# Performance work log

Measured on AMD Instinct MI355X. Metric: run time of the kernel, lower is better.

Reference implementation:

```python
import jax, jax.numpy as jnp
import numpy as np

EPS = 1e-12  # F.normalize eps


def _l2norm_c(x):
    # normalize over channel dim (axis=1), matching F.normalize(dim=1)
    n = jnp.sqrt(jnp.sum(x * x, axis=1, keepdims=True))
    return x / jnp.maximum(n, EPS)


def _rotate_all(q, angles_deg):
    """Rotate q [B,C,H,W] by every angle in angles_deg [A] via affine_grid +
    bilinear grid_sample (align_corners=False, zeros padding). Returns [A,B,C,H,W]."""
    B, C, H, W = q.shape
    th = jnp.deg2rad(angles_deg)
    # affine_grid align_corners=False output normalized coords
    xn = (2.0 * jnp.arange(W, dtype=q.dtype) + 1.0) / W - 1.0  # [W]
    yn = (2.0 * jnp.arange(H, dtype=q.dtype) + 1.0) / H - 1.0  # [H]
    c = jnp.cos(th)[:, None, None]
    s = jnp.sin(th)[:, None, None]
    gx = c * xn[None, None, :] - s * yn[None, :, None]  # [A,H,W]
    gy = s * xn[None, None, :] + c * yn[None, :, None]  # [A,H,W]
    # grid_sample align_corners=False: normalized -> input pixel coords
    ix = ((gx + 1.0) * W - 1.0) * 0.5
    iy = ((gy + 1.0) * H - 1.0) * 0.5
    x0 = jnp.floor(ix)
    y0 = jnp.floor(iy)
    wx = ix - x0  # frac weights
    wy = iy - y0
    x0i = x0.astype(jnp.int32)
    y0i = y0.astype(jnp.int32)

    def corner(yi, xi, w):
        valid = (xi >= 0) & (xi < W) & (yi >= 0) & (yi < H)  # zeros padding
        xc = jnp.clip(xi, 0, W - 1)
        yc = jnp.clip(yi, 0, H - 1)
        vals = q[:, :, yc, xc]  # advanced indexing -> [B,C,A,H,W]
        return vals * (w * valid.astype(q.dtype))[None, None]

    out = (corner(y0i, x0i, (1.0 - wx) * (1.0 - wy))
           + corner(y0i, x0i + 1, wx * (1.0 - wy))
           + corner(y0i + 1, x0i, (1.0 - wx) * wy)
           + corner(y0i + 1, x0i + 1, wx * wy))  # [B,C,A,H,W]
    return jnp.transpose(out, (2, 0, 1, 3, 4))  # [A,B,C,H,W]


def setup_inputs() -> dict:
    key = jax.random.key(0)
    ks = jax.random.split(key, 6)
    B, Cin, H, W, HID, A = 8, 768, 32, 32, 128, 36
    gallery_map = jax.random.normal(ks[0], (B, Cin, H, W), jnp.float32)
    query_map = jax.random.normal(ks[1], (B, Cin, H, W), jnp.float32)
    angles_deg = jnp.arange(A, dtype=jnp.float32) * 10.0 - 180.0
    Wg = jax.random.normal(ks[2], (HID, Cin), jnp.float32) / np.float32(np.sqrt(Cin))
    Wq = jax.random.normal(ks[3], (HID, Cin), jnp.float32) / np.float32(np.sqrt(Cin))
    W1 = jax.random.normal(ks[4], (HID, 4 * HID), jnp.float32) / np.float32(np.sqrt(4 * HID))
    b1 = jnp.zeros((HID,), jnp.float32)
    W2 = jax.random.normal(ks[5], (1, HID), jnp.float32) / np.float32(np.sqrt(HID))
    b2 = jnp.zeros((1,), jnp.float32)
    return {"gallery_map": gallery_map, "query_map": query_map, "Wg": Wg, "Wq": Wq,
            "W1": W1, "b1": b1, "W2": W2, "b2": b2, "angles_deg": angles_deg}


def reference(gallery_map, query_map, Wg, Wq, W1, b1, W2, b2, angles_deg):
    # 1x1-conv projections + channel L2 normalization (encode)
    g = _l2norm_c(jnp.einsum('oc,bchw->bohw', Wg, gallery_map))  # [B,HID,H,W]
    q = _l2norm_c(jnp.einsum('oc,bchw->bohw', Wq, query_map))    # [B,HID,H,W]
    qr = _rotate_all(q, angles_deg)  # [A,B,HID,H,W]
    HID = W1.shape[0]
    # head conv1 over cat([g, qr, g*qr, |g-qr|]) == sum of 4 block matmuls
    W1g, W1q, W1m, W1a = (W1[:, :HID], W1[:, HID:2 * HID],
                          W1[:, 2 * HID:3 * HID], W1[:, 3 * HID:])
    base = jnp.einsum('oc,bchw->bohw', W1g, g)  # angle-independent term
    h = (base[None]
         + jnp.einsum('oc,abchw->abohw', W1q, qr)
         + jnp.einsum('oc,abchw->abohw', W1m, g[None] * qr)
         + jnp.einsum('oc,abchw->abohw', W1a, jnp.abs(g[None] - qr))
         + b1[None, None, :, None, None])
    h = jax.nn.relu(h)  # [A,B,HID,H,W]
    H_, W_ = h.shape[-2], h.shape[-1]
    # head conv2 (HID->1) + spatial mean pool, per angle
    logits = jnp.einsum('c,abchw->ab', W2[0], h) / (H_ * W_) + b2[0]  # [A,B]
    return logits.T  # [B,A] matching torch.stack(logits, dim=1)
```

## Files before the change

kernel.cpp:

```cpp
#include <hip/hip_runtime.h>
#include <math.h>

#define B_   8
#define CIN  768
#define HID  128
#define NA   36
#define PP   1024

typedef _Float16 f16;
typedef __attribute__((ext_vector_type(2))) _Float16 f16x2;
typedef __attribute__((ext_vector_type(4))) _Float16 f16x4;
typedef __attribute__((ext_vector_type(8))) _Float16 f16x8;
typedef __attribute__((ext_vector_type(4))) float f32x4;

#define MFMA16(a, b, c) __builtin_amdgcn_mfma_f32_16x16x32_f16((a), (b), (c), 0, 0, 0)

__device__ inline f16x2 pkrtz(float a, float b) {
  union { __fp16 __attribute__((ext_vector_type(2))) r; f16x2 h; } u;
  u.r = __builtin_amdgcn_cvt_pkrtz(a, b);
  return u.h;
}

__device__ inline void rot_corners(float ct, float st, int y, int x,
                                   float w[4], int p[4]) {
  float xn = (2.0f * x + 1.0f) * (1.0f / 32.0f) - 1.0f;
  float yn = (2.0f * y + 1.0f) * (1.0f / 32.0f) - 1.0f;
  float gx = ct * xn - st * yn;
  float gy = st * xn + ct * yn;
  float ix = ((gx + 1.0f) * 32.0f - 1.0f) * 0.5f;
  float iy = ((gy + 1.0f) * 32.0f - 1.0f) * 0.5f;
  float x0f = floorf(ix), y0f = floorf(iy);
  float wx = ix - x0f, wy = iy - y0f;
  int x0 = (int)x0f, y0 = (int)y0f;
  int x1 = x0 + 1, y1 = y0 + 1;
  float vx0 = (x0 >= 0 && x0 < 32) ? 1.0f : 0.0f;
  float vx1 = (x1 >= 0 && x1 < 32) ? 1.0f : 0.0f;
  float vy0 = (y0 >= 0 && y0 < 32) ? 1.0f : 0.0f;
  float vy1 = (y1 >= 0 && y1 < 32) ? 1.0f : 0.0f;
  int cx0 = min(max(x0, 0), 31), cx1 = min(max(x1, 0), 31);
  int cy0 = min(max(y0, 0), 31), cy1 = min(max(y1, 0), 31);
  w[0] = (1.0f - wx) * (1.0f - wy) * vx0 * vy0;  p[0] = (cy0 << 5) + cx0;
  w[1] = wx * (1.0f - wy) * vx1 * vy0;           p[1] = (cy0 << 5) + cx1;
  w[2] = (1.0f - wx) * wy * vx0 * vy1;           p[2] = (cy1 << 5) + cx0;
  w[3] = wx * wy * vx1 * vy1;                    p[3] = (cy1 << 5) + cx1;
}

__global__ __launch_bounds__(256) void prep_k(
    const float* __restrict__ Wg, const float* __restrict__ Wq,
    const float* __restrict__ W1, const float* __restrict__ b2,
    f16* __restrict__ Wg_h, f16* __restrict__ Wq_h,
    f16* __restrict__ W1_h, float* __restrict__ out) {
  int idx = blockIdx.x * 256 + threadIdx.x;
  if (idx < B_ * NA) out[idx] = b2[0];
  if (idx < 32768) {
    int e = idx * 8;
    const float* src; f16* dst; int off;
    if (e < 98304)       { src = Wg; dst = Wg_h; off = e; }
    else if (e < 196608) { src = Wq; dst = Wq_h; off = e - 98304; }
    else                 { src = W1; dst = W1_h; off = e - 196608; }
    float4 lo = *(const float4*)(src + off);
    float4 hi = *(const float4*)(src + off + 4);
    f16x8 h;
    h[0] = (f16)lo.x; h[1] = (f16)lo.y; h[2] = (f16)lo.z; h[3] = (f16)lo.w;
    h[4] = (f16)hi.x; h[5] = (f16)hi.y; h[6] = (f16)hi.z; h[7] = (f16)hi.w;
    *(f16x8*)(dst + off) = h;
  }
}

__global__ __launch_bounds__(128) void proj_norm_k(
    const float* __restrict__ gal, const float* __restrict__ qry,
    const f16* __restrict__ Wg_h, const f16* __restrict__ Wq_h,
    f16* __restrict__ gout, f16* __restrict__ qout) {
  __shared__ f16 Ws[128 * 72];
  __shared__ f16 bounce[32 * 136];
  int pblk = blockIdx.x, b = blockIdx.y;
  const float* src = blockIdx.z ? qry : gal;
  const f16* Wm = blockIdx.z ? Wq_h : Wg_h;
  f16* dst = blockIdx.z ? qout : gout;
  int tid = threadIdx.x, lane = tid & 63, wv = tid >> 6;
  int q = lane >> 4, lr = lane & 15;
  int p0 = pblk * 32 + wv * 16;
  const float* imgB = src + (size_t)b * CIN * PP;
  f32x4 acc[8];
  #pragma unroll
  for (int t = 0; t < 8; t++) acc[t] = (f32x4){0.f, 0.f, 0.f, 0.f};

  for (int cc = 0; cc < CIN; cc += 64) {
    #pragma unroll
    for (int j = 0; j < 8; j++)
      *(f16x8*)&Ws[tid * 72 + j * 8] = *(const f16x8*)(Wm + tid * CIN + cc + j * 8);
    __syncthreads();
    #pragma unroll
    for (int ks = 0; ks < 64; ks += 32) {
      const float* ip = imgB + (size_t)(cc + ks + q * 8) * PP + p0 + lr;
      float v0 = ip[0], v1 = ip[PP], v2 = ip[2 * PP], v3 = ip[3 * PP];
      float v4 = ip[4 * PP], v5 = ip[5 * PP], v6 = ip[6 * PP], v7 = ip[7 * PP];
      union { f16x8 v; f16x2 h[4]; } bf;
      bf.h[0] = pkrtz(v0, v1);
      bf.h[1] = pkrtz(v2, v3);
      bf.h[2] = pkrtz(v4, v5);
      bf.h[3] = pkrtz(v6, v7);
      #pragma unroll
      for (int t = 0; t < 8; t++) {
        f16x8 af = *(const f16x8*)&Ws[(t * 16 + lr) * 72 + ks + q * 8];
        acc[t] = MFMA16(af, bf.v, acc[t]);
      }
    }
    __syncthreads();
  }
  float ss = 0.f;
  #pragma unroll
  for (int t = 0; t < 8; t++)
    #pragma unroll
    for (int r = 0; r < 4; r++) ss += acc[t][r] * acc[t][r];
  ss += __shfl_xor(ss, 16);
  ss += __shfl_xor(ss, 32);
  float inv = 1.0f / fmaxf(sqrtf(ss), 1e-12f);
  int prow = wv * 16 + lr;
  #pragma unroll
  for (int t = 0; t < 8; t++) {
    f16x4 h;
    h[0] = (f16)(acc[t][0] * inv); h[1] = (f16)(acc[t][1] * inv);
    h[2] = (f16)(acc[t][2] * inv); h[3] = (f16)(acc[t][3] * inv);
    *(f16x4*)&bounce[prow * 136 + t * 16 + q * 4] = h;
  }
  __syncthreads();
  int row = tid >> 2, seg = tid & 3;
  f16* gp = dst + (size_t)((b << 10) + pblk * 32 + row) * HID + seg * 32;
  #pragma unroll
  for (int j = 0; j < 4; j++)
    *(f16x8*)(gp + j * 8) = *(const f16x8*)&bounce[row * 136 + seg * 32 + j * 8];
}

__global__ __launch_bounds__(256) void posproj_k(
    const f16* __restrict__ g, const f16* __restrict__ W1_h,
    const float* __restrict__ b1, float* __restrict__ baseb1) {
  __shared__ f16 As[32 * 136];
  __shared__ f16 Wls[128 * 136];
  int b = blockIdx.x >> 5, y = blockIdx.x & 31;
  int tid = threadIdx.x, lane = tid & 63, wv = tid >> 6;
  int q = lane >> 4, lr = lane & 15;
  int nq = wv * 32;
  int pbase = (b << 10) + (y << 5);
  {
    int row = tid >> 3, col = (tid & 7) * 16;
    *(f16x8*)&As[row * 136 + col]     = *(const f16x8*)(g + (size_t)(pbase + row) * HID + col);
    *(f16x8*)&As[row * 136 + col + 8] = *(const f16x8*)(g + (size_t)(pbase + row) * HID + col + 8);
  }
  {
    int o = tid >> 1, half = (tid & 1) * 64;
    #pragma unroll
    for (int j = 0; j < 8; j++)
      *(f16x8*)&Wls[o * 136 + half + j * 8] = *(const f16x8*)(W1_h + o * 512 + half + j * 8);
  }
  __syncthreads();
  f32x4 acc[2][2];
  #pragma unroll
  for (int i = 0; i < 2; i++)
    #pragma unroll
    for (int j = 0; j < 2; j++) acc[i][j] = (f32x4){0.f, 0.f, 0.f, 0.f};
  #pragma unroll
  for (int k0 = 0; k0 < 128; k0 += 32) {
    f16x8 a0 = *(const f16x8*)&As[(lr) * 136 + k0 + q * 8];
    f16x8 a1 = *(const f16x8*)&As[(16 + lr) * 136 + k0 + q * 8];
    f16x8 b0 = *(const f16x8*)&Wls[(nq + lr) * 136 + k0 + q * 8];
    f16x8 b1v = *(const f16x8*)&Wls[(nq + 16 + lr) * 136 + k0 + q * 8];
    acc[0][0] = MFMA16(a0, b0, acc[0][0]); acc[0][1] = MFMA16(a0, b1v, acc[0][1]);
    acc[1][0] = MFMA16(a1, b0, acc[1][0]); acc[1][1] = MFMA16(a1, b1v, acc[1][1]);
  }
  #pragma unroll
  for (int mi = 0; mi < 2; mi++)
    #pragma unroll
    for (int r = 0; r < 4; r++) {
      int m = mi * 16 + q * 4 + r;
      #pragma unroll
      for (int ni = 0; ni < 2; ni++) {
        int n = nq + ni * 16 + lr;
        baseb1[(size_t)(pbase + m) * HID + n] = acc[mi][ni][r] + b1[n];
      }
    }
}

__global__ __launch_bounds__(256, 3) void main_k(
    const f16* __restrict__ g_h, const f16* __restrict__ q_h,
    const float* __restrict__ baseb1, const f16* __restrict__ W1_h,
    const float* __restrict__ W2, const float* __restrict__ angles,
    float* __restrict__ out) {
  __shared__ f16 Xs[32 * 392];
  __shared__ float redw[4];
  int y = blockIdx.x, b = blockIdx.y;
  int tid = threadIdx.x;
  int lane = tid & 63, wv = tid >> 6;
  int q = lane >> 4, lr = lane & 15;
  int nq = wv * 32;

  f16x8 bfr[12][2];
  #pragma unroll
  for (int s = 0; s < 12; s++)
    #pragma unroll
    for (int ni = 0; ni < 2; ni++) {
      int o = nq + ni * 16 + lr;
      bfr[s][ni] = *(const f16x8*)(W1_h + o * 512 + 128 + s * 32 + q * 8);
    }

  float bacc[2][2][4];
  float w2v[2];
  #pragma unroll
  for (int ni = 0; ni < 2; ni++) w2v[ni] = W2[nq + ni * 16 + lr];
  #pragma unroll
  for (int mi = 0; mi < 2; mi++)
    #pragma unroll
    for (int r = 0; r < 4; r++) {
      int m = mi * 16 + q * 4 + r;
      #pragma unroll
      for (int ni = 0; ni < 2; ni++)
        bacc[mi][ni][r] = baseb1[(size_t)((b << 10) + (y << 5) + m) * HID + nq + ni * 16 + lr];
    }

  int bx = tid >> 3, ks = tid & 7;
  const f16* qB = q_h + (size_t)(b << 10) * HID;
  const f16* gB = g_h + (size_t)((b << 10) + (y << 5) + bx) * HID;

  for (int it = 0; it < 6; it++) {
    int a = blockIdx.z * 6 + it;
    float th = angles[a] * 0.017453292519943295f;
    float ct = cosf(th), st = sinf(th);

    {
      float w4[4]; int p4[4];
      rot_corners(ct, st, y, bx, w4, p4);
      f16x2 wc[4];
      #pragma unroll
      for (int k = 0; k < 4; k++) {
        f16 h = (f16)w4[k];
        wc[k] = (f16x2){h, h};
      }
      const f16* c0p = qB + p4[0] * HID;
      const f16* c1p = qB + p4[1] * HID;
      const f16* c2p = qB + p4[2] * HID;
      const f16* c3p = qB + p4[3] * HID;
      #pragma unroll
      for (int cg = 0; cg < 2; cg++) {
        int c = ks * 16 + cg * 8;
        union U8 { f16x8 v; f16x2 h[4]; } u0, u1, u2, u3, gg, oq, om, oa;
        u0.v = *(const f16x8*)(c0p + c);
        u1.v = *(const f16x8*)(c1p + c);
        u2.v = *(const f16x8*)(c2p + c);
        u3.v = *(const f16x8*)(c3p + c);
        gg.v = *(const f16x8*)(gB + c);
        #pragma unroll
        for (int i = 0; i < 4; i++) {
          f16x2 qr = u0.h[i] * wc[0] + u1.h[i] * wc[1]
                   + u2.h[i] * wc[2] + u3.h[i] * wc[3];
          f16x2 mm = gg.h[i] * qr;
          union { f16x2 h; unsigned int u; } dd;
          dd.h = gg.h[i] - qr;
          dd.u &= 0x7fff7fffu;
          oq.h[i] = qr; om.h[i] = mm; oa.h[i] = dd.h;
        }
        *(f16x8*)&Xs[bx * 392 + c] = oq.v;
        *(f16x8*)&Xs[bx * 392 + 128 + c] = om.v;
        *(f16x8*)&Xs[bx * 392 + 256 + c] = oa.v;
      }
    }
    __syncthreads();

    f32x4 acc[2][2];
    #pragma unroll
    for (int i = 0; i < 2; i++)
      #pragma unroll
      for (int j = 0; j < 2; j++) acc[i][j] = (f32x4){0.f, 0.f, 0.f, 0.f};
    #pragma unroll
    for (int s = 0; s < 12; s++) {
      f16x8 a0 = *(const f16x8*)&Xs[(lr) * 392 + s * 32 + q * 8];
      f16x8 a1 = *(const f16x8*)&Xs[(16 + lr) * 392 + s * 32 + q * 8];
      acc[0][0] = MFMA16(a0, bfr[s][0], acc[0][0]);
      acc[0][1] = MFMA16(a0, bfr[s][1], acc[0][1]);
      acc[1][0] = MFMA16(a1, bfr[s][0], acc[1][0]);
      acc[1][1] = MFMA16(a1, bfr[s][1], acc[1][1]);
    }

    float s = 0.f;
    #pragma unroll
    for (int mi = 0; mi < 2; mi++)
      #pragma unroll
      for (int ni = 0; ni < 2; ni++)
        #pragma unroll
        for (int r = 0; r < 4; r++)
          s = fmaf(w2v[ni], fmaxf(acc[mi][ni][r] + bacc[mi][ni][r], 0.f), s);
    #pragma unroll
    for (int off = 32; off > 0; off >>= 1) s += __shfl_down(s, off, 64);
    if (lane == 0) redw[wv] = s;
    __syncthreads();
    if (tid == 0) {
      float tot = redw[0] + redw[1] + redw[2] + redw[3];
      atomicAdd(&out[b * NA + a], tot * (1.0f / 1024.0f));
    }
  }
}

extern "C" void kernel_launch(void* const* d_in, const int* in_sizes, int n_in,
                              void* d_out, int out_size, void* d_ws, size_t ws_size,
                              hipStream_t stream) {
  const float* gal = (const float*)d_in[0];
  const float* qry = (const float*)d_in[1];
  const float* Wg  = (const float*)d_in[2];
  const float* Wq  = (const float*)d_in[3];
  const float* W1  = (const float*)d_in[4];
  const float* b1  = (const float*)d_in[5];
  const float* W2  = (const float*)d_in[6];
  const float* b2  = (const float*)d_in[7];
  const float* ang = (const float*)d_in[8];
  float* out = (float*)d_out;
  char* ws = (char*)d_ws;
  f16*   g_h    = (f16*)ws;
  f16*   q_h    = (f16*)(ws + (2u << 20));
  float* baseb1 = (float*)(ws + (4u << 20));
  f16*   Wg_h   = (f16*)(ws + (8u << 20));
  f16*   Wq_h   = (f16*)(ws + (8u << 20) + 196608);
  f16*   W1_h   = (f16*)(ws + (8u << 20) + 393216);

  hipLaunchKernelGGL(prep_k, dim3(128), dim3(256), 0, stream,
                     Wg, Wq, W1, b2, Wg_h, Wq_h, W1_h, out);
  hipLaunchKernelGGL(proj_norm_k, dim3(32, 8, 2), dim3(128), 0, stream,
                     gal, qry, Wg_h, Wq_h, g_h, q_h);
  hipLaunchKernelGGL(posproj_k, dim3(256), dim3(256), 0, stream,
                     g_h, W1_h, b1, baseb1);
  hipLaunchKernelGGL(main_k, dim3(32, 8, 6), dim3(256), 0, stream,
                     g_h, q_h, baseb1, W1_h, W2, ang, out);
}
```

Baseline: 174.7 us.

## Fuse projection and base-term kernels; split-K projection; double-buffer angle tiles

Merges the projection/normalize kernel and the base-term GEMM into one 512-thread kernel. Each block now splits the 768-channel reduction across four wave groups and reduces the partials through shared memory before normalizing. The gallery-side blocks then compute the W1g·g + b1 term directly from the normalized tile in LDS, removing one launch and a global reread. In the main kernel the per-angle staging buffer is double-buffered, which drops the second per-angle barrier, and the six angle reductions are batched into one final barrier with six atomics. The cost is much larger shared memory per block and more work on the z==0 blocks.

```diff
diff --git a/kernel.cpp b/kernel.cpp
--- a/kernel.cpp
+++ b/kernel.cpp
@@ -67,118 +67,115 @@
   }
 }
 
-__global__ __launch_bounds__(128) void proj_norm_k(
+#define WCH_S 264
+#define PS_S  132
+#define GN_S  136
+__global__ __launch_bounds__(512, 4) void projfused_k(
     const float* __restrict__ gal, const float* __restrict__ qry,
     const f16* __restrict__ Wg_h, const f16* __restrict__ Wq_h,
-    f16* __restrict__ gout, f16* __restrict__ qout) {
-  __shared__ f16 Ws[128 * 72];
-  __shared__ f16 bounce[32 * 136];
-  int pblk = blockIdx.x, b = blockIdx.y;
-  const float* src = blockIdx.z ? qry : gal;
-  const f16* Wm = blockIdx.z ? Wq_h : Wg_h;
-  f16* dst = blockIdx.z ? qout : gout;
+    const f16* __restrict__ W1_h, const float* __restrict__ b1,
+    f16* __restrict__ gout, f16* __restrict__ qout,
+    float* __restrict__ baseb1) {
+  __shared__ __align__(16) char LDSU[67584];
+  f16*   Wch = (f16*)LDSU;
+  float* ps  = (float*)LDSU;
+  f16*   Gn  = (f16*)LDSU;
+  f16*   W1l = (f16*)(LDSU + 8704);
+
+  int pblk = blockIdx.x, b = blockIdx.y, z = blockIdx.z;
+  const float* imgB = (z ? qry : gal) + (size_t)b * CIN * PP;
+  const f16* Wm = z ? Wq_h : Wg_h;
+  f16* dst = z ? qout : gout;
   int tid = threadIdx.x, lane = tid & 63, wv = tid >> 6;
   int q = lane >> 4, lr = lane & 15;
-  int p0 = pblk * 32 + wv * 16;
-  const float* imgB = src + (size_t)b * CIN * PP;
+  int kw = wv & 3, mw = wv >> 2;
+  int pw = pblk * 32 + mw * 16;
+
   f32x4 acc[8];
   #pragma unroll
   for (int t = 0; t < 8; t++) acc[t] = (f32x4){0.f, 0.f, 0.f, 0.f};
 
-  for (int cc = 0; cc < CIN; cc += 64) {
+  int so = tid >> 2, sseg = (tid & 3) * 64;
+  for (int cc = 0; cc < CIN; cc += 256) {
     #pragma unroll
     for (int j = 0; j < 8; j++)
-      *(f16x8*)&Ws[tid * 72 + j * 8] = *(const f16x8*)(Wm + tid * CIN + cc + j * 8);
-    __syncthreads();
-    #pragma unroll
-    for (int ks = 0; ks < 64; ks += 32) {
-      const float* ip = imgB + (size_t)(cc + ks + q * 8) * PP + p0 + lr;
+      *(f16x8*)&Wch[so * WCH_S + sseg + j * 8] =
+          *(const f16x8*)(Wm + so * CIN + cc + sseg + j * 8);
+    __syncthreads();
+    #pragma unroll
+    for (int ks = 0; ks < 2; ks++) {
+      int k0 = kw * 64 + ks * 32;
+      const float* ip = imgB + (size_t)(cc + k0 + q * 8) * PP + pw + lr;
       float v0 = ip[0], v1 = ip[PP], v2 = ip[2 * PP], v3 = ip[3 * PP];
       float v4 = ip[4 * PP], v5 = ip[5 * PP], v6 = ip[6 * PP], v7 = ip[7 * PP];
       union { f16x8 v; f16x2 h[4]; } bf;
-      bf.h[0] = pkrtz(v0, v1);
-      bf.h[1] = pkrtz(v2, v3);
-      bf.h[2] = pkrtz(v4, v5);
-      bf.h[3] = pkrtz(v6, v7);
-      #pragma unroll
-      for (int t = 0; t < 8; t++) {
-        f16x8 af = *(const f16x8*)&Ws[(t * 16 + lr) * 72 + ks + q * 8];
-        acc[t] = MFMA16(af, bf.v, acc[t]);
+      bf.h[0] = pkrtz(v0, v1); bf.h[1] = pkrtz(v2, v3);
+      bf.h[2] = pkrtz(v4, v5); bf.h[3] = pkrtz(v6, v7);
+      #pragma unroll
+      for (int og = 0; og < 8; og++) {
+        f16x8 af = *(const f16x8*)&Wch[(og * 16 + lr) * WCH_S + k0 + q * 8];
+        acc[og] = MFMA16(af, bf.v, acc[og]);
       }
     }
     __syncthreads();
   }
-  float ss = 0.f;
-  #pragma unroll
-  for (int t = 0; t < 8; t++)
-    #pragma unroll
-    for (int r = 0; r < 4; r++) ss += acc[t][r] * acc[t][r];
-  ss += __shfl_xor(ss, 16);
-  ss += __shfl_xor(ss, 32);
+
+  #pragma unroll
+  for (int og = 0; og < 8; og++)
+    *(f32x4*)&ps[kw * (32 * PS_S) + (mw * 16 + lr) * PS_S + og * 16 + q * 4] = acc[og];
+  __syncthreads();
+  int pos = tid >> 4, oo = (tid & 15) * 8;
+  f32x4 v0s = (f32x4){0.f,0.f,0.f,0.f}, v1s = (f32x4){0.f,0.f,0.f,0.f};
+  #pragma unroll
+  for (int k = 0; k < 4; k++) {
+    v0s += *(const f32x4*)&ps[k * (32 * PS_S) + pos * PS_S + oo];
+    v1s += *(const f32x4*)&ps[k * (32 * PS_S) + pos * PS_S + oo + 4];
+  }
+  float ss = v0s.x*v0s.x + v0s.y*v0s.y + v0s.z*v0s.z + v0s.w*v0s.w
+           + v1s.x*v1s.x + v1s.y*v1s.y + v1s.z*v1s.z + v1s.w*v1s.w;
+  ss += __shfl_xor(ss, 1); ss += __shfl_xor(ss, 2);
+  ss += __shfl_xor(ss, 4); ss += __shfl_xor(ss, 8);
   float inv = 1.0f / fmaxf(sqrtf(ss), 1e-12f);
-  int prow = wv * 16 + lr;
-  #pragma unroll
-  for (int t = 0; t < 8; t++) {
-    f16x4 h;
-    h[0] = (f16)(acc[t][0] * inv); h[1] = (f16)(acc[t][1] * inv);
-    h[2] = (f16)(acc[t][2] * inv); h[3] = (f16)(acc[t][3] * inv);
-    *(f16x4*)&bounce[prow * 136 + t * 16 + q * 4] = h;
-  }
-  __syncthreads();
-  int row = tid >> 2, seg = tid & 3;
-  f16* gp = dst + (size_t)((b << 10) + pblk * 32 + row) * HID + seg * 32;
-  #pragma unroll
-  for (int j = 0; j < 4; j++)
-    *(f16x8*)(gp + j * 8) = *(const f16x8*)&bounce[row * 136 + seg * 32 + j * 8];
-}
-
-__global__ __launch_bounds__(256) void posproj_k(
-    const f16* __restrict__ g, const f16* __restrict__ W1_h,
-    const float* __restrict__ b1, float* __restrict__ baseb1) {
-  __shared__ f16 As[32 * 136];
-  __shared__ f16 Wls[128 * 136];
-  int b = blockIdx.x >> 5, y = blockIdx.x & 31;
-  int tid = threadIdx.x, lane = tid & 63, wv = tid >> 6;
-  int q = lane >> 4, lr = lane & 15;
-  int nq = wv * 32;
-  int pbase = (b << 10) + (y << 5);
-  {
-    int row = tid >> 3, col = (tid & 7) * 16;
-    *(f16x8*)&As[row * 136 + col]     = *(const f16x8*)(g + (size_t)(pbase + row) * HID + col);
-    *(f16x8*)&As[row * 136 + col + 8] = *(const f16x8*)(g + (size_t)(pbase + row) * HID + col + 8);
-  }
-  {
-    int o = tid >> 1, half = (tid & 1) * 64;
-    #pragma unroll
-    for (int j = 0; j < 8; j++)
-      *(f16x8*)&Wls[o * 136 + half + j * 8] = *(const f16x8*)(W1_h + o * 512 + half + j * 8);
-  }
-  __syncthreads();
-  f32x4 acc[2][2];
-  #pragma unroll
-  for (int i = 0; i < 2; i++)
-    #pragma unroll
-    for (int j = 0; j < 2; j++) acc[i][j] = (f32x4){0.f, 0.f, 0.f, 0.f};
-  #pragma unroll
-  for (int k0 = 0; k0 < 128; k0 += 32) {
-    f16x8 a0 = *(const f16x8*)&As[(lr) * 136 + k0 + q * 8];
-    f16x8 a1 = *(const f16x8*)&As[(16 + lr) * 136 + k0 + q * 8];
-    f16x8 b0 = *(const f16x8*)&Wls[(nq + lr) * 136 + k0 + q * 8];
-    f16x8 b1v = *(const f16x8*)&Wls[(nq + 16 + lr) * 136 + k0 + q * 8];
-    acc[0][0] = MFMA16(a0, b0, acc[0][0]); acc[0][1] = MFMA16(a0, b1v, acc[0][1]);
-    acc[1][0] = MFMA16(a1, b0, acc[1][0]); acc[1][1] = MFMA16(a1, b1v, acc[1][1]);
-  }
-  #pragma unroll
-  for (int mi = 0; mi < 2; mi++)
-    #pragma unroll
-    for (int r = 0; r < 4; r++) {
-      int m = mi * 16 + q * 4 + r;
-      #pragma unroll
-      for (int ni = 0; ni < 2; ni++) {
-        int n = nq + ni * 16 + lr;
-        baseb1[(size_t)(pbase + m) * HID + n] = acc[mi][ni][r] + b1[n];
+  f16x8 gn8;
+  gn8[0] = (f16)(v0s.x*inv); gn8[1] = (f16)(v0s.y*inv);
+  gn8[2] = (f16)(v0s.z*inv); gn8[3] = (f16)(v0s.w*inv);
+  gn8[4] = (f16)(v1s.x*inv); gn8[5] = (f16)(v1s.y*inv);
+  gn8[6] = (f16)(v1s.z*inv); gn8[7] = (f16)(v1s.w*inv);
+  *(f16x8*)(dst + (size_t)((b << 10) + pblk * 32 + pos) * HID + oo) = gn8;
+
+  if (z == 0) {
+    __syncthreads();
+    *(f16x8*)&Gn[pos * GN_S + oo] = gn8;
+    {
+      int o = tid >> 2, seg = (tid & 3) * 32;
+      #pragma unroll
+      for (int j = 0; j < 4; j++)
+        *(f16x8*)&W1l[o * GN_S + seg + j * 8] =
+            *(const f16x8*)(W1_h + o * 512 + seg + j * 8);
+    }
+    __syncthreads();
+    int nw = wv & 3, mw2 = wv >> 2;
+    f32x4 acc2[2];
+    acc2[0] = (f32x4){0.f,0.f,0.f,0.f}; acc2[1] = (f32x4){0.f,0.f,0.f,0.f};
+    #pragma unroll
+    for (int ks = 0; ks < 4; ks++) {
+      f16x8 bfv = *(const f16x8*)&Gn[(mw2 * 16 + lr) * GN_S + ks * 32 + q * 8];
+      #pragma unroll
+      for (int og2 = 0; og2 < 2; og2++) {
+        f16x8 af = *(const f16x8*)&W1l[(nw * 32 + og2 * 16 + lr) * GN_S + ks * 32 + q * 8];
+        acc2[og2] = MFMA16(af, bfv, acc2[og2]);
       }
     }
+    #pragma unroll
+    for (int og2 = 0; og2 < 2; og2++) {
+      int o0 = nw * 32 + og2 * 16 + q * 4;
+      float4 bb = *(const float4*)(b1 + o0);
+      float4 r;
+      r.x = acc2[og2][0] + bb.x; r.y = acc2[og2][1] + bb.y;
+      r.z = acc2[og2][2] + bb.z; r.w = acc2[og2][3] + bb.w;
+      *(float4*)(baseb1 + (size_t)((b << 10) + pblk * 32 + mw2 * 16 + lr) * HID + o0) = r;
+    }
+  }
 }
 
 __global__ __launch_bounds__(256, 3) void main_k(
@@ -186,8 +183,8 @@
     const float* __restrict__ baseb1, const f16* __restrict__ W1_h,
     const float* __restrict__ W2, const float* __restrict__ angles,
     float* __restrict__ out) {
-  __shared__ f16 Xs[32 * 392];
-  __shared__ float redw[4];
+  __shared__ f16 Xs[2][32 * 392];
+  __shared__ float redl[24];
   int y = blockIdx.x, b = blockIdx.y;
   int tid = threadIdx.x;
   int lane = tid & 63, wv = tid >> 6;
@@ -221,10 +218,13 @@
   const f16* qB = q_h + (size_t)(b << 10) * HID;
   const f16* gB = g_h + (size_t)((b << 10) + (y << 5) + bx) * HID;
 
+  float spart[6];
+
   for (int it = 0; it < 6; it++) {
     int a = blockIdx.z * 6 + it;
     float th = angles[a] * 0.017453292519943295f;
     float ct = cosf(th), st = sinf(th);
+    f16* Xb = &Xs[it & 1][0];
 
     {
       float w4[4]; int p4[4];
@@ -258,9 +258,9 @@
           dd.u &= 0x7fff7fffu;
           oq.h[i] = qr; om.h[i] = mm; oa.h[i] = dd.h;
         }
-        *(f16x8*)&Xs[bx * 392 + c] = oq.v;
-        *(f16x8*)&Xs[bx * 392 + 128 + c] = om.v;
-        *(f16x8*)&Xs[bx * 392 + 256 + c] = oa.v;
+        *(f16x8*)&Xb[bx * 392 + c] = oq.v;
+        *(f16x8*)&Xb[bx * 392 + 128 + c] = om.v;
+        *(f16x8*)&Xb[bx * 392 + 256 + c] = oa.v;
       }
     }
     __syncthreads();
@@ -272,8 +272,8 @@
       for (int j = 0; j < 2; j++) acc[i][j] = (f32x4){0.f, 0.f, 0.f, 0.f};
     #pragma unroll
     for (int s = 0; s < 12; s++) {
-      f16x8 a0 = *(const f16x8*)&Xs[(lr) * 392 + s * 32 + q * 8];
-      f16x8 a1 = *(const f16x8*)&Xs[(16 + lr) * 392 + s * 32 + q * 8];
+      f16x8 a0 = *(const f16x8*)&Xb[(lr) * 392 + s * 32 + q * 8];
+      f16x8 a1 = *(const f16x8*)&Xb[(16 + lr) * 392 + s * 32 + q * 8];
       acc[0][0] = MFMA16(a0, bfr[s][0], acc[0][0]);
       acc[0][1] = MFMA16(a0, bfr[s][1], acc[0][1]);
       acc[1][0] = MFMA16(a1, bfr[s][0], acc[1][0]);
@@ -288,14 +288,20 @@
         #pragma unroll
         for (int r = 0; r < 4; r++)
           s = fmaf(w2v[ni], fmaxf(acc[mi][ni][r] + bacc[mi][ni][r], 0.f), s);
-    #pragma unroll
-    for (int off = 32; off > 0; off >>= 1) s += __shfl_down(s, off, 64);
-    if (lane == 0) redw[wv] = s;
-    __syncthreads();
-    if (tid == 0) {
-      float tot = redw[0] + redw[1] + redw[2] + redw[3];
-      atomicAdd(&out[b * NA + a], tot * (1.0f / 1024.0f));
-    }
+    spart[it] = s;
+  }
+
+  #pragma unroll
+  for (int it = 0; it < 6; it++) {
+    float v = spart[it];
+    #pragma unroll
+    for (int off = 32; off > 0; off >>= 1) v += __shfl_down(v, off, 64);
+    if (lane == 0) redl[wv * 6 + it] = v;
+  }
+  __syncthreads();
+  if (tid < 6) {
+    float tot = redl[tid] + redl[6 + tid] + redl[12 + tid] + redl[18 + tid];
+    atomicAdd(&out[b * NA + blockIdx.z * 6 + tid], tot * (1.0f / 1024.0f));
   }
 }
 
@@ -322,10 +328,8 @@
 
   hipLaunchKernelGGL(prep_k, dim3(128), dim3(256), 0, stream,
                      Wg, Wq, W1, b2, Wg_h, Wq_h, W1_h, out);
-  hipLaunchKernelGGL(proj_norm_k, dim3(32, 8, 2), dim3(128), 0, stream,
-                     gal, qry, Wg_h, Wq_h, g_h, q_h);
-  hipLaunchKernelGGL(posproj_k, dim3(256), dim3(256), 0, stream,
-                     g_h, W1_h, b1, baseb1);
+  hipLaunchKernelGGL(projfused_k, dim3(32, 8, 2), dim3(512), 0, stream,
+                     gal, qry, Wg_h, Wq_h, W1_h, b1, g_h, q_h, baseb1);
   hipLaunchKernelGGL(main_k, dim3(32, 8, 6), dim3(256), 0, stream,
                      g_h, q_h, baseb1, W1_h, W2, ang, out);
 }
```

Result: faster. 167.6 us (-4.1%).
